# Kernel optimization log

Hardware: AMD Instinct MI355X
Metric: run time of the kernel (lower is better)

The kernel has to match this reference:

```python
import jax, jax.numpy as jnp
import numpy as np

B, S, D, H, FF = 4, 2048, 768, 12, 3072
DH = D // H
EPS = 1e-5
NEG = -1e18


def setup_inputs() -> dict:
    key = jax.random.key(0)
    ks = jax.random.split(key, 12)
    xavier = lambda k, fi, fo: jax.random.uniform(k, (fi, fo), jnp.float32,
                                                  -np.sqrt(6.0 / (fi + fo)), np.sqrt(6.0 / (fi + fo)))
    return {
        "x": jax.random.normal(ks[0], (B, S, D), jnp.float32),
        "mask": jax.random.bernoulli(ks[1], 0.1, (B, S, S)),  # True = masked
        "wq": xavier(ks[2], D, D),
        "wk": xavier(ks[3], D, D),
        "wv": xavier(ks[4], D, D),
        "wo": xavier(ks[5], D, D),
        "bo": jnp.zeros((D,), jnp.float32),
        "w1": xavier(ks[6], D, FF),
        "w2": xavier(ks[7], FF, D),
        "g1": jnp.ones((D,), jnp.float32),
        "b1": jnp.zeros((D,), jnp.float32),
        "g2": jnp.ones((D,), jnp.float32),
        "b2": jnp.zeros((D,), jnp.float32),
    }


def _layernorm(x, g, b):
    mu = jnp.mean(x, axis=-1, keepdims=True)
    var = jnp.mean(jnp.square(x - mu), axis=-1, keepdims=True)
    return (x - mu) * jax.lax.rsqrt(var + EPS) * g + b


def reference(x, mask, wq, wk, wv, wo, bo, w1, w2, g1, b1, g2, b2):
    # --- self-attention sublayer (pre-LN) ---
    h = _layernorm(x, g1, b1)
    split = lambda t: t.reshape(B, S, H, DH).transpose(0, 2, 1, 3)  # [B,H,S,DH]
    q = split(h @ wq) / np.sqrt(DH)
    k = split(h @ wk)
    v = split(h @ wv)
    scores = jnp.einsum('bhqd,bhkd->bhqk', q, k)
    scores = jnp.where(mask[:, None, :, :], NEG, scores)
    weights = jax.nn.softmax(scores, axis=-1)
    ctx = jnp.einsum('bhqk,bhkd->bhqd', weights, v)
    ctx = ctx.transpose(0, 2, 1, 3).reshape(B, S, D)
    x = x + (ctx @ wo + bo)
    # --- feed-forward sublayer (pre-LN) ---
    h = _layernorm(x, g2, b2)
    y = jax.nn.relu(h @ w1) @ w2
    return x + y
```

## Files before the change

### kernel.cpp

```cpp
#include <hip/hip_runtime.h>
#include <cstdint>


typedef __bf16 bf16_t;
typedef __bf16 bf16x8 __attribute__((ext_vector_type(8)));
typedef __bf16 bf16x4 __attribute__((ext_vector_type(4)));
typedef __bf16 bf16x2 __attribute__((ext_vector_type(2)));
typedef float  f32x4  __attribute__((ext_vector_type(4)));
typedef float  f32x16 __attribute__((ext_vector_type(16)));

#define LOG2E 1.44269504088896340736f

__device__ __forceinline__ float exp2_fast(float x) {
  float r;
  asm("v_exp_f32 %0, %1" : "=v"(r) : "v"(x));
  return r;
}

__device__ __forceinline__ f32x4 mfma16(bf16x8 a, bf16x8 b, f32x4 c) {
  return __builtin_amdgcn_mfma_f32_16x16x32_bf16(a, b, c, 0, 0, 0);
}
__device__ __forceinline__ f32x16 mfma32(bf16x8 a, bf16x8 b, f32x16 c) {
  return __builtin_amdgcn_mfma_f32_32x32x16_bf16(a, b, c, 0, 0, 0);
}

__device__ __forceinline__ void gload16(const bf16_t* gsrc, bf16_t* lds) {
  __builtin_amdgcn_global_load_lds(
      (const __attribute__((address_space(1))) unsigned int*)(uintptr_t)gsrc,
      (__attribute__((address_space(3))) unsigned int*)(uintptr_t)lds,
      16, 0, 0);
}

__device__ __forceinline__ unsigned pk2(float a, float b) {
  bf16x2 v = {(bf16_t)a, (bf16_t)b};
  return __builtin_bit_cast(unsigned, v);
}
__device__ __forceinline__ void pl32_swap(unsigned& a, unsigned& b) {
  asm("v_permlane32_swap_b32 %0, %1" : "+v"(a), "+v"(b));
}
__device__ __forceinline__ bf16x8 frag4(unsigned w0, unsigned w1,
                                        unsigned w2, unsigned w3) {
  union { unsigned u[4]; bf16x8 v; } t;
  t.u[0] = w0; t.u[1] = w1; t.u[2] = w2; t.u[3] = w3;
  return t.v;
}

__global__ __launch_bounds__(256) void prep_weights(
    const float* __restrict__ wq, const float* __restrict__ wk,
    const float* __restrict__ wv, const float* __restrict__ wo,
    const float* __restrict__ w1, const float* __restrict__ w2,
    bf16_t* __restrict__ dst)
{
  __shared__ float tile[32][33];
  const int id = blockIdx.x;
  const float* W; size_t doff; int K, N, tx, local; float scale = 1.f;
  if (id < 576)       { W = wq; doff = 0;       K = 768;  N = 768;  tx = 24; local = id;        scale = 0.125f * LOG2E; }
  else if (id < 1152) { W = wk; doff = 589824;  K = 768;  N = 768;  tx = 24; local = id - 576;  }
  else if (id < 1728) { W = wv; doff = 1179648; K = 768;  N = 768;  tx = 24; local = id - 1152; }
  else if (id < 2304) { W = wo; doff = 1769472; K = 768;  N = 768;  tx = 24; local = id - 1728; }
  else if (id < 4608) { W = w1; doff = 2359296; K = 768;  N = 3072; tx = 96; local = id - 2304; }
  else                { W = w2; doff = 4718592; K = 3072; N = 768;  tx = 24; local = id - 4608; }
  const int n0 = (local % tx) * 32, k0 = (local / tx) * 32;
  const int tx_ = threadIdx.x, ty_ = threadIdx.y;
#pragma unroll
  for (int i = 0; i < 32; i += 8)
    tile[ty_ + i][tx_] = W[(size_t)(k0 + ty_ + i) * N + n0 + tx_];
  __syncthreads();
  bf16_t* const Wt = dst + doff;
#pragma unroll
  for (int i = 0; i < 32; i += 8)
    Wt[(size_t)(n0 + ty_ + i) * K + k0 + tx_] = (bf16_t)(tile[tx_][ty_ + i] * scale);
}

__global__ __launch_bounds__(256) void pack_mask(
    const int* __restrict__ mask, unsigned int* __restrict__ bits)
{
  const int gid4 = blockIdx.x * 256 + threadIdx.x;
  const int4 v = ((const int4*)mask)[gid4];
  unsigned nib = (v.x != 0 ? 1u : 0u) | (v.y != 0 ? 2u : 0u) |
                 (v.z != 0 ? 4u : 0u) | (v.w != 0 ? 8u : 0u);
  nib <<= ((threadIdx.x & 7) * 4);
  nib |= __shfl_xor((int)nib, 1, 64);
  nib |= __shfl_xor((int)nib, 2, 64);
  nib |= __shfl_xor((int)nib, 4, 64);
  if ((threadIdx.x & 7) == 0) bits[gid4 >> 3] = nib;
}

__global__ __launch_bounds__(256) void ln_kernel(
    const float* __restrict__ xin, const float* __restrict__ gamma,
    const float* __restrict__ beta, bf16_t* __restrict__ outb)
{
  const int w = threadIdx.x >> 6, lane = threadIdx.x & 63;
  const int row = blockIdx.x * 4 + w;
  const float* xr = xin + (size_t)row * 768;
  float4 v[3];
  float s = 0.f, s2 = 0.f;
#pragma unroll
  for (int p = 0; p < 3; ++p) {
    v[p] = *(const float4*)(xr + p * 256 + lane * 4);
    s  += v[p].x + v[p].y + v[p].z + v[p].w;
    s2 += v[p].x * v[p].x + v[p].y * v[p].y + v[p].z * v[p].z + v[p].w * v[p].w;
  }
#pragma unroll
  for (int m = 1; m <= 32; m <<= 1) {
    s  += __shfl_xor(s, m, 64);
    s2 += __shfl_xor(s2, m, 64);
  }
  const float mu  = s * (1.0f / 768.0f);
  const float var = s2 * (1.0f / 768.0f) - mu * mu;
  const float rs  = rsqrtf(var + 1e-5f);
  bf16_t* orow = outb + (size_t)row * 768;
#pragma unroll
  for (int p = 0; p < 3; ++p) {
    const float4 g4 = *(const float4*)(gamma + p * 256 + lane * 4);
    const float4 b4 = *(const float4*)(beta  + p * 256 + lane * 4);
    bf16x4 o = {(bf16_t)((v[p].x - mu) * rs * g4.x + b4.x),
                (bf16_t)((v[p].y - mu) * rs * g4.y + b4.y),
                (bf16_t)((v[p].z - mu) * rs * g4.z + b4.z),
                (bf16_t)((v[p].w - mu) * rs * g4.w + b4.w)};
    *(bf16x4*)(orow + p * 256 + lane * 4) = o;
  }
}

template <bool RELU, bool OUT_F32, bool HAS_BIAS, bool HAS_RES, bool VOUT>
__global__ __launch_bounds__(256) void gemm_kernel(
    const bf16_t* __restrict__ A, const bf16_t* __restrict__ Bt,
    void* __restrict__ Cout, const float* __restrict__ bias,
    const float* __restrict__ res, int Mdim, int Ndim, int Kdim,
    bf16_t* __restrict__ vout)
{
  __shared__ __align__(16) bf16_t Smem[2][2][128 * 64];
  const int tid = threadIdx.x;
  const int lane = tid & 63, w = tid >> 6;
  const int l15 = lane & 15, g = lane >> 4;
  const int gx = gridDim.x;
  const int nwg = gx * gridDim.y;
  const int p = blockIdx.y * gx + blockIdx.x;
  const int wg = (p & 7) * (nwg >> 3) + (p >> 3);
  const int bm = (wg / gx) * 128, bn = (wg % gx) * 128;
  const int wr = (w >> 1) * 64, wc = (w & 1) * 64;
  const int swz = l15 & 7;

  auto STAGE = [&](int kt, int buf) {
    const int k0 = kt << 6;
    bf16_t* const as = Smem[buf][0];
    bf16_t* const bs = Smem[buf][1];
#pragma unroll
    for (int it = 0; it < 4; ++it) {
      const int ch = it * 256 + tid;
      const int r = ch >> 3, c = ch & 7;
      gload16(A + (size_t)(bm + r) * Kdim + k0 + ((c ^ (r & 7)) * 8), as + ch * 8);
    }
#pragma unroll
    for (int it = 0; it < 4; ++it) {
      const int ch = it * 256 + tid;
      const int r = ch >> 3, c = ch & 7;
      gload16(Bt + (size_t)(bn + r) * Kdim + k0 + ((c ^ (r & 7)) * 8), bs + ch * 8);
    }
  };

  f32x4 acc[4][4] = {};
  const int nK = Kdim >> 6;
  STAGE(0, 0);
  __syncthreads();
  for (int kt = 0; kt < nK; ++kt) {
    const int cur = kt & 1;
    if (kt + 1 < nK) STAGE(kt + 1, cur ^ 1);
    const bf16_t* const As = Smem[cur][0];
    const bf16_t* const Bs = Smem[cur][1];
#pragma unroll
    for (int kk = 0; kk < 2; ++kk) {
      bf16x8 af[4], bfr[4];
#pragma unroll
      for (int i = 0; i < 4; ++i)
        af[i] = *(const bf16x8*)(As + (wr + i * 16 + l15) * 64 +
                                 (((kk * 4 + g) ^ swz) * 8));
#pragma unroll
      for (int j = 0; j < 4; ++j)
        bfr[j] = *(const bf16x8*)(Bs + (wc + j * 16 + l15) * 64 +
                                  (((kk * 4 + g) ^ swz) * 8));
#pragma unroll
      for (int i = 0; i < 4; ++i)
#pragma unroll
        for (int j = 0; j < 4; ++j)
          acc[i][j] = mfma16(af[i], bfr[j], acc[i][j]);
    }
    __syncthreads();
  }

  if constexpr (!OUT_F32) {
    bf16_t* const wb = &Smem[0][0][0] + w * 4096;
    if (VOUT && bn >= 1536) {
#pragma unroll
      for (int i = 0; i < 4; ++i)
#pragma unroll
        for (int j = 0; j < 4; ++j)
#pragma unroll
          for (int r = 0; r < 4; ++r) {
            const int srow = i * 16 + g * 4 + r;
            const int d = j * 16 + l15;
            *(bf16_t*)((char*)wb + d * 128 + ((srow * 2) ^ ((d & 7) << 4))) =
                (bf16_t)acc[i][j][r];
          }
      __syncthreads();
      const int b = bm >> 11;
      const int h = (bn + wc - 1536) >> 6;
      const int s0 = (bm & 2047) + wr;
      const int c = lane & 7;
#pragma unroll
      for (int ps = 0; ps < 8; ++ps) {
        const int drow = (lane >> 3) + ps * 8;
        bf16x8 v = *(const bf16x8*)((char*)wb + drow * 128 +
                                    ((c * 16) ^ ((drow & 7) << 4)));
        *(bf16x8*)(vout + ((size_t)((b * 12 + h) * 64 + drow)) * 2048 +
                   s0 + c * 8) = v;
      }
    } else {
#pragma unroll
      for (int i = 0; i < 4; ++i)
#pragma unroll
        for (int j = 0; j < 4; ++j)
#pragma unroll
          for (int r = 0; r < 4; ++r) {
            const int row = i * 16 + g * 4 + r, col = j * 16 + l15;
            float v = acc[i][j][r];
            if constexpr (RELU) v = fmaxf(v, 0.f);
            *(bf16_t*)((char*)wb + row * 128 + ((col * 2) ^ ((row & 7) << 4))) =
                (bf16_t)v;
          }
      __syncthreads();
      bf16_t* const crow0 = (bf16_t*)Cout + (size_t)(bm + wr) * Ndim + bn + wc;
      const int c = lane & 7;
#pragma unroll
      for (int ps = 0; ps < 8; ++ps) {
        const int row = (lane >> 3) + ps * 8;
        bf16x8 v = *(const bf16x8*)((char*)wb + row * 128 +
                                    ((c * 16) ^ ((row & 7) << 4)));
        *(bf16x8*)(crow0 + (size_t)row * Ndim + c * 8) = v;
      }
    }
  } else {
    float* const fb = (float*)&Smem[0][0][0] + w * 2048;
    const int c = lane & 7;
#pragma unroll
    for (int jh = 0; jh < 2; ++jh) {
      if (jh) __syncthreads();
#pragma unroll
      for (int i = 0; i < 4; ++i)
#pragma unroll
        for (int jj = 0; jj < 2; ++jj)
#pragma unroll
          for (int r = 0; r < 4; ++r) {
            const int row = i * 16 + g * 4 + r, col = jj * 16 + l15;
            *(float*)((char*)fb + row * 128 + ((col * 4) ^ ((row & 7) << 4))) =
                acc[i][jh * 2 + jj][r];
          }
      __syncthreads();
      const int gcol = bn + wc + jh * 32 + c * 4;
      float4 bv = {0.f, 0.f, 0.f, 0.f};
      if constexpr (HAS_BIAS) bv = *(const float4*)(bias + gcol);
#pragma unroll
      for (int ps = 0; ps < 8; ++ps) {
        const int row = (lane >> 3) + ps * 8;
        float4 v = *(const float4*)((char*)fb + row * 128 +
                                    ((c * 16) ^ ((row & 7) << 4)));
        if constexpr (HAS_BIAS) { v.x += bv.x; v.y += bv.y; v.z += bv.z; v.w += bv.w; }
        if constexpr (HAS_RES) {
          const float4 rv = *(const float4*)(res + (size_t)(bm + wr + row) * Ndim + gcol);
          v.x += rv.x; v.y += rv.y; v.z += rv.z; v.w += rv.w;
        }
        *(float4*)((float*)Cout + (size_t)(bm + wr + row) * Ndim + gcol) = v;
      }
    }
  }
}

__global__ __launch_bounds__(256, 4) void attn_kernel(
    const bf16_t* __restrict__ qkv, const bf16_t* __restrict__ vT,
    const unsigned int* __restrict__ mbits, bf16_t* __restrict__ ctx)
{
  __shared__ __align__(16) bf16_t KsBuf[2][64 * 64];
  __shared__ __align__(16) bf16_t VsBuf[2][64 * 64];
  const int tid = threadIdx.x;
  const int lane = tid & 63, w = tid >> 6;
  const int q32 = lane & 31, hi = lane >> 5;
  const int bh = blockIdx.x;
  const int qt = blockIdx.y;
  const int b = bh / 12, h = bh % 12;
  const int qabs = qt * 128 + w * 32 + q32;

  bf16x8 qf[4];
#pragma unroll
  for (int c = 0; c < 4; ++c)
    qf[c] = *(const bf16x8*)(qkv + (size_t)(b * 2048 + qabs) * 2304 +
                             h * 64 + c * 16 + hi * 8);

  auto stage = [&](bf16_t* ks, bf16_t* vs, int kt) {
    const size_t kb0 = (size_t)(b * 2048 + kt * 64);
#pragma unroll
    for (int it = 0; it < 2; ++it) {
      const int ch = it * 256 + tid;
      const int r = ch >> 3, c = ch & 7;
      gload16(qkv + (kb0 + r) * 2304 + 768 + h * 64 + ((c ^ (r & 7)) * 8), ks + ch * 8);
    }
#pragma unroll
    for (int it = 0; it < 2; ++it) {
      const int ch = it * 256 + tid;
      const int r = ch >> 3, c = ch & 7;
      gload16(vT + (size_t)(bh * 64 + r) * 2048 + kt * 64 + ((c ^ (r & 7)) * 8),
              vs + ch * 8);
    }
  };

  f32x16 oacc[2] = {};
  float lr0 = 0.f, lr1 = 0.f, lr2 = 0.f, lr3 = 0.f;

  stage(KsBuf[0], VsBuf[0], 0);
  __syncthreads();

  for (int kt = 0; kt < 32; ++kt) {
    const bf16_t* ksc = (kt & 1) ? KsBuf[1] : KsBuf[0];
    const bf16_t* vsc = (kt & 1) ? VsBuf[1] : VsBuf[0];
    if (kt < 31)
      stage((kt & 1) ? KsBuf[0] : KsBuf[1], (kt & 1) ? VsBuf[0] : VsBuf[1], kt + 1);

    const uint2 mm = *(const uint2*)(mbits + (size_t)(b * 2048 + qabs) * 64 + kt * 2);
    const unsigned mwv[2] = {mm.x >> (hi * 4), mm.y >> (hi * 4)};

    f32x16 sacc[2] = {};
#pragma unroll
    for (int c = 0; c < 4; ++c) {
#pragma unroll
      for (int kb = 0; kb < 2; ++kb) {
        const int row = kb * 32 + q32;
        const int slot = (2 * c + hi) ^ (row & 7);
        bf16x8 kf = *(const bf16x8*)(ksc + row * 64 + slot * 8);
        sacc[kb] = mfma32(kf, qf[c], sacc[kb]);
      }
    }

#pragma unroll
    for (int kb = 0; kb < 2; ++kb) {
#pragma unroll
      for (int rq = 0; rq < 4; ++rq) {
        const unsigned sel = mwv[kb] >> (8 * rq);
        {
          const float e0 = exp2_fast(sacc[kb][rq * 4 + 0]);
          const float p0 = (sel & 1u) ? 0.f : e0;
          sacc[kb][rq * 4 + 0] = p0;  lr0 += p0;
          const float e1 = exp2_fast(sacc[kb][rq * 4 + 1]);
          const float p1 = ((sel >> 1) & 1u) ? 0.f : e1;
          sacc[kb][rq * 4 + 1] = p1;  lr1 += p1;
          const float e2 = exp2_fast(sacc[kb][rq * 4 + 2]);
          const float p2 = ((sel >> 2) & 1u) ? 0.f : e2;
          sacc[kb][rq * 4 + 2] = p2;  lr2 += p2;
          const float e3 = exp2_fast(sacc[kb][rq * 4 + 3]);
          const float p3 = ((sel >> 3) & 1u) ? 0.f : e3;
          sacc[kb][rq * 4 + 3] = p3;  lr3 += p3;
        }
      }
    }

    __builtin_amdgcn_s_setprio(1);
#pragma unroll
    for (int kb = 0; kb < 2; ++kb) {
      unsigned u0 = pk2(sacc[kb][0],  sacc[kb][1]);
      unsigned u1 = pk2(sacc[kb][2],  sacc[kb][3]);
      unsigned u2 = pk2(sacc[kb][4],  sacc[kb][5]);
      unsigned u3 = pk2(sacc[kb][6],  sacc[kb][7]);
      unsigned u4 = pk2(sacc[kb][8],  sacc[kb][9]);
      unsigned u5 = pk2(sacc[kb][10], sacc[kb][11]);
      unsigned u6 = pk2(sacc[kb][12], sacc[kb][13]);
      unsigned u7 = pk2(sacc[kb][14], sacc[kb][15]);
      pl32_swap(u0, u2);  pl32_swap(u1, u3);
      pl32_swap(u4, u6);  pl32_swap(u5, u7);
      bf16x8 p0 = frag4(u0, u1, u2, u3);
      bf16x8 p1 = frag4(u4, u5, u6, u7);
#pragma unroll
      for (int ks = 0; ks < 2; ++ks) {
        const bf16x8 pf = ks ? p1 : p0;
        const int cg = kb * 4 + ks * 2 + hi;
#pragma unroll
        for (int dt = 0; dt < 2; ++dt) {
          const int row = dt * 32 + q32;
          bf16x8 vf = *(const bf16x8*)(vsc + row * 64 + ((cg ^ (row & 7)) * 8));
          oacc[dt] = mfma32(vf, pf, oacc[dt]);
        }
      }
    }
    __builtin_amdgcn_s_setprio(0);
    __syncthreads();
  }

  float lrun = (lr0 + lr1) + (lr2 + lr3);
  lrun += __shfl_xor(lrun, 32, 64);
  const float inv = (lrun > 0.f) ? 1.f / lrun : 0.f;
  bf16_t* crow = ctx + (size_t)(b * 2048 + qabs) * 768 + h * 64;
#pragma unroll
  for (int dt = 0; dt < 2; ++dt)
#pragma unroll
    for (int rq = 0; rq < 4; ++rq) {
      bf16x4 ov = {(bf16_t)(oacc[dt][rq * 4 + 0] * inv),
                   (bf16_t)(oacc[dt][rq * 4 + 1] * inv),
                   (bf16_t)(oacc[dt][rq * 4 + 2] * inv),
                   (bf16_t)(oacc[dt][rq * 4 + 3] * inv)};
      *(bf16x4*)(crow + dt * 32 + rq * 8 + hi * 4) = ov;
    }
}

extern "C" void kernel_launch(void* const* d_in, const int* in_sizes, int n_in,
                              void* d_out, int out_size, void* d_ws, size_t ws_size,
                              hipStream_t stream) {
  const float* x  = (const float*)d_in[0];
  const int* mask = (const int*)d_in[1];
  const float* wq = (const float*)d_in[2];
  const float* wk = (const float*)d_in[3];
  const float* wv = (const float*)d_in[4];
  const float* wo = (const float*)d_in[5];
  const float* bo = (const float*)d_in[6];
  const float* w1 = (const float*)d_in[7];
  const float* w2 = (const float*)d_in[8];
  const float* g1 = (const float*)d_in[9];
  const float* b1 = (const float*)d_in[10];
  const float* g2 = (const float*)d_in[11];
  const float* b2 = (const float*)d_in[12];
  float* out = (float*)d_out;

  char* p = (char*)d_ws;
  bf16_t* WQKVT = (bf16_t*)p; p += (size_t)2304 * 768 * 2;
  bf16_t* WOT   = (bf16_t*)p; p += (size_t)768 * 768 * 2;
  bf16_t* W1T   = (bf16_t*)p; p += (size_t)3072 * 768 * 2;
  bf16_t* W2T   = (bf16_t*)p; p += (size_t)768 * 3072 * 2;
  unsigned int* MB = (unsigned int*)p; p += (size_t)4 * 2048 * 64 * 4;
  bf16_t* Hbuf  = (bf16_t*)p; p += (size_t)8192 * 768 * 2;
  float*  X2    = (float*)p;  p += (size_t)8192 * 768 * 4;
  bf16_t* QKV   = (bf16_t*)p; p += (size_t)8192 * 2304 * 2;
  bf16_t* CTX   = (bf16_t*)p;
  bf16_t* FFN   = QKV;
  bf16_t* VT    = (bf16_t*)X2;

  prep_weights<<<6912, dim3(32, 8), 0, stream>>>(wq, wk, wv, wo, w1, w2, WQKVT);
  pack_mask<<<16384, 256, 0, stream>>>(mask, MB);

  ln_kernel<<<2048, 256, 0, stream>>>(x, g1, b1, Hbuf);
  gemm_kernel<false, false, false, false, true><<<dim3(18, 64), 256, 0, stream>>>(
      Hbuf, WQKVT, QKV, nullptr, nullptr, 8192, 2304, 768, VT);
  attn_kernel<<<dim3(48, 16), 256, 0, stream>>>(QKV, VT, MB, CTX);
  gemm_kernel<false, true, true, true, false><<<dim3(6, 64), 256, 0, stream>>>(
      CTX, WOT, X2, bo, x, 8192, 768, 768, nullptr);

  ln_kernel<<<2048, 256, 0, stream>>>(X2, g2, b2, Hbuf);
  gemm_kernel<true, false, false, false, false><<<dim3(24, 64), 256, 0, stream>>>(
      Hbuf, W1T, FFN, nullptr, nullptr, 8192, 3072, 768, nullptr);
  gemm_kernel<false, true, false, true, false><<<dim3(6, 64), 256, 0, stream>>>(
      FFN, W2T, out, nullptr, X2, 8192, 768, 3072, nullptr);
}
```

Before: 254.6 us.

## Use 128x64 tiles for N=768 GEMMs and fuse mask packing into weight prep

Parameterises the GEMM kernel's N tile width and uses 64-wide tiles for the output-projection and FFN-down GEMMs, doubling their workgroup count to fix the wave-quantization tail on many CUs. Mask bit-packing is merged into the weight preparation kernel as extra blocks, removing one kernel launch. Smaller N tiles reduce operand reuse per workgroup, increasing A-matrix reloads.

Measured after the change: 255.3 us. Within noise of the previous version (+0.3%).

```diff
diff --git a/kernel.cpp b/kernel.cpp
--- a/kernel.cpp
+++ b/kernel.cpp
@@ -45,12 +45,26 @@
   return t.v;
 }
 
-__global__ __launch_bounds__(256) void prep_weights(
+__global__ __launch_bounds__(256) void prep_all(
     const float* __restrict__ wq, const float* __restrict__ wk,
     const float* __restrict__ wv, const float* __restrict__ wo,
     const float* __restrict__ w1, const float* __restrict__ w2,
-    bf16_t* __restrict__ dst)
+    bf16_t* __restrict__ dst,
+    const int* __restrict__ mask, unsigned int* __restrict__ bits)
 {
+  if (blockIdx.x >= 6912) {
+    const int t = threadIdx.y * 32 + threadIdx.x;
+    const int gid4 = (blockIdx.x - 6912) * 256 + t;
+    const int4 v = ((const int4*)mask)[gid4];
+    unsigned nib = (v.x != 0 ? 1u : 0u) | (v.y != 0 ? 2u : 0u) |
+                   (v.z != 0 ? 4u : 0u) | (v.w != 0 ? 8u : 0u);
+    nib <<= ((t & 7) * 4);
+    nib |= __shfl_xor((int)nib, 1, 64);
+    nib |= __shfl_xor((int)nib, 2, 64);
+    nib |= __shfl_xor((int)nib, 4, 64);
+    if ((t & 7) == 0) bits[gid4 >> 3] = nib;
+    return;
+  }
   __shared__ float tile[32][33];
   const int id = blockIdx.x;
   const float* W; size_t doff; int K, N, tx, local; float scale = 1.f;
@@ -72,20 +86,6 @@
     Wt[(size_t)(n0 + ty_ + i) * K + k0 + tx_] = (bf16_t)(tile[tx_][ty_ + i] * scale);
 }
 
-__global__ __launch_bounds__(256) void pack_mask(
-    const int* __restrict__ mask, unsigned int* __restrict__ bits)
-{
-  const int gid4 = blockIdx.x * 256 + threadIdx.x;
-  const int4 v = ((const int4*)mask)[gid4];
-  unsigned nib = (v.x != 0 ? 1u : 0u) | (v.y != 0 ? 2u : 0u) |
-                 (v.z != 0 ? 4u : 0u) | (v.w != 0 ? 8u : 0u);
-  nib <<= ((threadIdx.x & 7) * 4);
-  nib |= __shfl_xor((int)nib, 1, 64);
-  nib |= __shfl_xor((int)nib, 2, 64);
-  nib |= __shfl_xor((int)nib, 4, 64);
-  if ((threadIdx.x & 7) == 0) bits[gid4 >> 3] = nib;
-}
-
 __global__ __launch_bounds__(256) void ln_kernel(
     const float* __restrict__ xin, const float* __restrict__ gamma,
     const float* __restrict__ beta, bf16_t* __restrict__ outb)
@@ -122,14 +122,16 @@
   }
 }
 
-template <bool RELU, bool OUT_F32, bool HAS_BIAS, bool HAS_RES, bool VOUT>
+template <bool RELU, bool OUT_F32, bool HAS_BIAS, bool HAS_RES, bool VOUT, int BNT>
 __global__ __launch_bounds__(256) void gemm_kernel(
     const bf16_t* __restrict__ A, const bf16_t* __restrict__ Bt,
     void* __restrict__ Cout, const float* __restrict__ bias,
     const float* __restrict__ res, int Mdim, int Ndim, int Kdim,
     bf16_t* __restrict__ vout)
 {
-  __shared__ __align__(16) bf16_t Smem[2][2][128 * 64];
+  constexpr int WCW = BNT / 2;
+  constexpr int NJ  = WCW / 16;
+  __shared__ __align__(16) bf16_t Smem[2 * (128 + BNT) * 64];
   const int tid = threadIdx.x;
   const int lane = tid & 63, w = tid >> 6;
   const int l15 = lane & 15, g = lane >> 4;
@@ -137,14 +139,14 @@
   const int nwg = gx * gridDim.y;
   const int p = blockIdx.y * gx + blockIdx.x;
   const int wg = (p & 7) * (nwg >> 3) + (p >> 3);
-  const int bm = (wg / gx) * 128, bn = (wg % gx) * 128;
-  const int wr = (w >> 1) * 64, wc = (w & 1) * 64;
+  const int bm = (wg / gx) * 128, bn = (wg % gx) * BNT;
+  const int wr = (w >> 1) * 64, wc = (w & 1) * WCW;
   const int swz = l15 & 7;
 
   auto STAGE = [&](int kt, int buf) {
     const int k0 = kt << 6;
-    bf16_t* const as = Smem[buf][0];
-    bf16_t* const bs = Smem[buf][1];
+    bf16_t* const as = Smem + buf * (128 + BNT) * 64;
+    bf16_t* const bs = as + 128 * 64;
 #pragma unroll
     for (int it = 0; it < 4; ++it) {
       const int ch = it * 256 + tid;
@@ -152,49 +154,49 @@
       gload16(A + (size_t)(bm + r) * Kdim + k0 + ((c ^ (r & 7)) * 8), as + ch * 8);
     }
 #pragma unroll
-    for (int it = 0; it < 4; ++it) {
+    for (int it = 0; it < BNT / 32; ++it) {
       const int ch = it * 256 + tid;
       const int r = ch >> 3, c = ch & 7;
       gload16(Bt + (size_t)(bn + r) * Kdim + k0 + ((c ^ (r & 7)) * 8), bs + ch * 8);
     }
   };
 
-  f32x4 acc[4][4] = {};
+  f32x4 acc[4][NJ] = {};
   const int nK = Kdim >> 6;
   STAGE(0, 0);
   __syncthreads();
   for (int kt = 0; kt < nK; ++kt) {
     const int cur = kt & 1;
     if (kt + 1 < nK) STAGE(kt + 1, cur ^ 1);
-    const bf16_t* const As = Smem[cur][0];
-    const bf16_t* const Bs = Smem[cur][1];
+    const bf16_t* const As = Smem + cur * (128 + BNT) * 64;
+    const bf16_t* const Bs = As + 128 * 64;
 #pragma unroll
     for (int kk = 0; kk < 2; ++kk) {
-      bf16x8 af[4], bfr[4];
+      bf16x8 af[4], bfr[NJ];
 #pragma unroll
       for (int i = 0; i < 4; ++i)
         af[i] = *(const bf16x8*)(As + (wr + i * 16 + l15) * 64 +
                                  (((kk * 4 + g) ^ swz) * 8));
 #pragma unroll
-      for (int j = 0; j < 4; ++j)
+      for (int j = 0; j < NJ; ++j)
         bfr[j] = *(const bf16x8*)(Bs + (wc + j * 16 + l15) * 64 +
                                   (((kk * 4 + g) ^ swz) * 8));
 #pragma unroll
       for (int i = 0; i < 4; ++i)
 #pragma unroll
-        for (int j = 0; j < 4; ++j)
+        for (int j = 0; j < NJ; ++j)
           acc[i][j] = mfma16(af[i], bfr[j], acc[i][j]);
     }
     __syncthreads();
   }
 
   if constexpr (!OUT_F32) {
-    bf16_t* const wb = &Smem[0][0][0] + w * 4096;
+    bf16_t* const wb = Smem + w * 4096;
     if (VOUT && bn >= 1536) {
 #pragma unroll
       for (int i = 0; i < 4; ++i)
 #pragma unroll
-        for (int j = 0; j < 4; ++j)
+        for (int j = 0; j < NJ; ++j)
 #pragma unroll
           for (int r = 0; r < 4; ++r) {
             const int srow = i * 16 + g * 4 + r;
@@ -219,7 +221,7 @@
 #pragma unroll
       for (int i = 0; i < 4; ++i)
 #pragma unroll
-        for (int j = 0; j < 4; ++j)
+        for (int j = 0; j < NJ; ++j)
 #pragma unroll
           for (int r = 0; r < 4; ++r) {
             const int row = i * 16 + g * 4 + r, col = j * 16 + l15;
@@ -240,10 +242,10 @@
       }
     }
   } else {
-    float* const fb = (float*)&Smem[0][0][0] + w * 2048;
+    float* const fb = (float*)Smem + w * 2048;
     const int c = lane & 7;
 #pragma unroll
-    for (int jh = 0; jh < 2; ++jh) {
+    for (int jh = 0; jh < WCW / 32; ++jh) {
       if (jh) __syncthreads();
 #pragma unroll
       for (int i = 0; i < 4; ++i)
@@ -439,19 +441,19 @@
   bf16_t* FFN   = QKV;
   bf16_t* VT    = (bf16_t*)X2;
 
-  prep_weights<<<6912, dim3(32, 8), 0, stream>>>(wq, wk, wv, wo, w1, w2, WQKVT);
-  pack_mask<<<16384, 256, 0, stream>>>(mask, MB);
+  prep_all<<<6912 + 16384, dim3(32, 8), 0, stream>>>(
+      wq, wk, wv, wo, w1, w2, WQKVT, mask, MB);
 
   ln_kernel<<<2048, 256, 0, stream>>>(x, g1, b1, Hbuf);
-  gemm_kernel<false, false, false, false, true><<<dim3(18, 64), 256, 0, stream>>>(
+  gemm_kernel<false, false, false, false, true, 128><<<dim3(18, 64), 256, 0, stream>>>(
       Hbuf, WQKVT, QKV, nullptr, nullptr, 8192, 2304, 768, VT);
   attn_kernel<<<dim3(48, 16), 256, 0, stream>>>(QKV, VT, MB, CTX);
-  gemm_kernel<false, true, true, true, false><<<dim3(6, 64), 256, 0, stream>>>(
+  gemm_kernel<false, true, true, true, false, 64><<<dim3(12, 64), 256, 0, stream>>>(
       CTX, WOT, X2, bo, x, 8192, 768, 768, nullptr);
 
   ln_kernel<<<2048, 256, 0, stream>>>(X2, g2, b2, Hbuf);
-  gemm_kernel<true, false, false, false, false><<<dim3(24, 64), 256, 0, stream>>>(
+  gemm_kernel<true, false, false, false, false, 128><<<dim3(24, 64), 256, 0, stream>>>(
       Hbuf, W1T, FFN, nullptr, nullptr, 8192, 3072, 768, nullptr);
-  gemm_kernel<false, true, false, true, false><<<dim3(6, 64), 256, 0, stream>>>(
+  gemm_kernel<false, true, false, true, false, 64><<<dim3(12, 64), 256, 0, stream>>>(
       FFN, W2T, out, nullptr, X2, 8192, 768, 3072, nullptr);
 }
```
